# Performance work log

Hardware: AMD Instinct MI355X
Metric: run time of the kernel (lower is better)

Reference implementation:

```python
import jax, jax.numpy as jnp
import numpy as np

B = 4096
LATENT, COND, HIDDEN, OUT, E, GATE_H = 768, 512, 1024, 512, 8, 512
INPUT = LATENT + COND          # 1280
INTER = LATENT + HIDDEN        # 1792
NEG_SLOPE = 0.01
LN_EPS = 1e-5


def _uniform(k, shape, bound):
    return jax.random.uniform(k, shape, jnp.float32, -bound, bound)


def setup_inputs() -> dict:
    key = jax.random.key(0)
    ks = jax.random.split(key, 32)
    inp = {
        'z': jax.random.normal(ks[0], (B, LATENT), jnp.float32),
        'c': jax.random.normal(ks[1], (B, COND), jnp.float32),
    }
    # expert weight/bias stacks, 'origin' init: stdv = 1/sqrt(wdim1)
    dims = [(INPUT, HIDDEN), (INTER, HIDDEN), (INTER, HIDDEN), (INTER, HIDDEN), (INTER, OUT)]
    ki = 2
    for i, (d1, d2) in enumerate(dims):
        stdv = 1.0 / np.sqrt(d1)
        inp[f'w{i}'] = _uniform(ks[ki], (E, d1, d2), stdv); ki += 1
        inp[f'b{i}'] = _uniform(ks[ki], (E, d2), stdv); ki += 1
        # LayerNorm params (torch default: gamma=1, beta=0)
        ln_dim = INPUT if i == 0 else INTER
        inp[f'ln_g{i}'] = jnp.ones((ln_dim,), jnp.float32)
        inp[f'ln_b{i}'] = jnp.zeros((ln_dim,), jnp.float32)
    # gate MLP: Linear(INPUT,GATE_H) -> LeakyReLU -> Linear(GATE_H,GATE_H) -> LeakyReLU -> Linear(GATE_H,E)
    for j, (fi, fo) in enumerate([(INPUT, GATE_H), (GATE_H, GATE_H), (GATE_H, E)]):
        bound = 1.0 / np.sqrt(fi)
        inp[f'gW{j}'] = _uniform(ks[ki], (fi, fo), bound); ki += 1
        inp[f'gb{j}'] = _uniform(ks[ki], (fo,), bound); ki += 1
    return inp


def _layernorm(x, g, b):
    mu = jnp.mean(x, axis=-1, keepdims=True)
    var = jnp.mean(jnp.square(x - mu), axis=-1, keepdims=True)
    return (x - mu) * jax.lax.rsqrt(var + LN_EPS) * g + b


def _mix(coeff, x, w, b):
    # per-sample soft-mixed expert linear: einsum('be,bj,ejk->bk') + einsum('be,ek->bk')
    h = jnp.einsum('bj,ejk->bek', x, w)          # [B,E,K]
    return jnp.einsum('be,bek->bk', coeff, h) + coeff @ b


def reference(z, c, w0, b0, w1, b1, w2, b2, w3, b3, w4, b4,
              ln_g0, ln_b0, ln_g1, ln_b1, ln_g2, ln_b2, ln_g3, ln_b3, ln_g4, ln_b4,
              gW0, gb0, gW1, gb1, gW2, gb2):
    zc = jnp.concatenate([z, c], axis=-1)        # [B, INPUT]
    g = jax.nn.leaky_relu(zc @ gW0 + gb0, NEG_SLOPE)
    g = jax.nn.leaky_relu(g @ gW1 + gb1, NEG_SLOPE)
    coeff = jax.nn.softmax(g @ gW2 + gb2, axis=-1)   # [B, E]

    x = _layernorm(zc, ln_g0, ln_b0)
    layer_out = jax.nn.leaky_relu(_mix(coeff, x, w0, b0), NEG_SLOPE)

    for w, b, lg, lb in [(w1, b1, ln_g1, ln_b1), (w2, b2, ln_g2, ln_b2), (w3, b3, ln_g3, ln_b3)]:
        x = _layernorm(jnp.concatenate([z, layer_out], axis=-1), lg, lb)
        layer_out = jax.nn.leaky_relu(layer_out + _mix(coeff, x, w, b), NEG_SLOPE)

    x = _layernorm(jnp.concatenate([z, layer_out], axis=-1), ln_g4, ln_b4)
    return _mix(coeff, x, w4, b4)                # [B, OUT], no residual/activation
```

## Files before the change

kernel.cpp:

```cpp
#include <hip/hip_runtime.h>


typedef _Float16 f16;
typedef _Float16 f16x8 __attribute__((ext_vector_type(8)));
typedef _Float16 f16x4 __attribute__((ext_vector_type(4)));
typedef float    f32x4 __attribute__((ext_vector_type(4)));

typedef __attribute__((address_space(1))) void as1_void;
typedef __attribute__((address_space(3))) void as3_void;

__device__ __forceinline__ void gload_lds16(const void* g, void* l) {
  __builtin_amdgcn_global_load_lds((as1_void*)g, (as3_void*)l, 16, 0, 0);
}

__device__ __forceinline__ float leaky(float v) { return v > 0.f ? v : 0.01f * v; }

__global__ __launch_bounds__(256) void transpose_cast(const float* __restrict__ in,
                                                      f16* __restrict__ out,
                                                      int R, int C) {
  __shared__ float tile[32][33];
  const size_t mat = (size_t)R * C;
  const float* I = in + mat * blockIdx.z;
  f16* O = out + mat * blockIdx.z;
  const int c0 = blockIdx.x * 32, r0 = blockIdx.y * 32;
  const int tx = threadIdx.x, ty = threadIdx.y;
#pragma unroll
  for (int i = ty; i < 32; i += 8)
    tile[i][tx] = I[(size_t)(r0 + i) * C + (c0 + tx)];
  __syncthreads();
#pragma unroll
  for (int i = ty; i < 32; i += 8)
    O[(size_t)(c0 + i) * R + (r0 + tx)] = (f16)tile[tx][i];
}

__global__ __launch_bounds__(256) void ln0_kernel(
    const float* __restrict__ z, const float* __restrict__ prev,
    const float* __restrict__ gam, const float* __restrict__ bet,
    f16* __restrict__ Xh, f16* __restrict__ raw) {
  constexpr int DP = 512, D = 768 + DP, NCH = D / 4;
  constexpr float invD = 1.f / (float)D;
  const int row = blockIdx.x, tid = threadIdx.x;
  const float4* z4 = (const float4*)(z + (size_t)row * 768);
  const float4* p4 = (const float4*)(prev + (size_t)row * DP);

  float4 v0 = (tid < 192) ? z4[tid] : p4[tid - 192];
  const bool has1 = (tid + 256) < NCH;
  float4 v1 = make_float4(0.f, 0.f, 0.f, 0.f);
  if (has1) v1 = p4[tid + 64];
  float s  = v0.x + v0.y + v0.z + v0.w + v1.x + v1.y + v1.z + v1.w;
  float ss = v0.x * v0.x + v0.y * v0.y + v0.z * v0.z + v0.w * v0.w +
             v1.x * v1.x + v1.y * v1.y + v1.z * v1.z + v1.w * v1.w;
#pragma unroll
  for (int off = 32; off > 0; off >>= 1) {
    s += __shfl_down(s, off);
    ss += __shfl_down(ss, off);
  }
  __shared__ float red[10];
  const int wave = tid >> 6, lane = tid & 63;
  if (lane == 0) { red[wave] = s; red[4 + wave] = ss; }
  __syncthreads();
  if (tid == 0) {
    float S = red[0] + red[1] + red[2] + red[3];
    float SS = red[4] + red[5] + red[6] + red[7];
    float mu = S * invD;
    float var = SS * invD - mu * mu;
    red[8] = mu;
    red[9] = rsqrtf(var + 1e-5f);
  }
  __syncthreads();
  const float mu = red[8], rs = red[9];
  {
    const int c = tid;
    float4 g4 = ((const float4*)gam)[c];
    float4 b4 = ((const float4*)bet)[c];
    f16x4 h;
    h[0] = (f16)((v0.x - mu) * rs * g4.x + b4.x);
    h[1] = (f16)((v0.y - mu) * rs * g4.y + b4.y);
    h[2] = (f16)((v0.z - mu) * rs * g4.z + b4.z);
    h[3] = (f16)((v0.w - mu) * rs * g4.w + b4.w);
    ((f16x4*)Xh)[(size_t)row * NCH + c] = h;
    f16x4 r;
    r[0] = (f16)v0.x; r[1] = (f16)v0.y; r[2] = (f16)v0.z; r[3] = (f16)v0.w;
    ((f16x4*)raw)[(size_t)row * NCH + c] = r;
  }
  if (has1) {
    const int c = tid + 256;
    float4 g4 = ((const float4*)gam)[c];
    float4 b4 = ((const float4*)bet)[c];
    f16x4 h;
    h[0] = (f16)((v1.x - mu) * rs * g4.x + b4.x);
    h[1] = (f16)((v1.y - mu) * rs * g4.y + b4.y);
    h[2] = (f16)((v1.z - mu) * rs * g4.z + b4.z);
    h[3] = (f16)((v1.w - mu) * rs * g4.w + b4.w);
    ((f16x4*)Xh)[(size_t)row * NCH + c] = h;
    f16x4 r;
    r[0] = (f16)v1.x; r[1] = (f16)v1.y; r[2] = (f16)v1.z; r[3] = (f16)v1.w;
    ((f16x4*)raw)[(size_t)row * NCH + c] = r;
  }
}

template <bool HAS_RESID>
__global__ __launch_bounds__(256) void ln_combine_kernel(
    const float* __restrict__ z, const f16* __restrict__ P,
    float* __restrict__ lay,
    const float* __restrict__ gam, const float* __restrict__ bet,
    f16* __restrict__ Xh) {
  constexpr int DP = 1024, D = 768 + DP, NCH = D / 4;
  constexpr size_t PSTRIDE = (size_t)4096 * DP;
  constexpr float invD = 1.f / (float)D;
  const int row = blockIdx.x, tid = threadIdx.x;
  const float4* z4 = (const float4*)(z + (size_t)row * 768);
  float4* lay4 = (float4*)(lay + (size_t)row * DP);

  auto comb = [&](int j) -> float4 {
    float4 v = make_float4(0.f, 0.f, 0.f, 0.f);
#pragma unroll
    for (int zz = 0; zz < 4; ++zz) {
      f16x4 a = ((const f16x4*)(P + PSTRIDE * zz + (size_t)row * DP))[j];
      v.x += (float)a[0]; v.y += (float)a[1]; v.z += (float)a[2]; v.w += (float)a[3];
    }
    if constexpr (HAS_RESID) {
      float4 r = lay4[j];
      v.x += r.x; v.y += r.y; v.z += r.z; v.w += r.w;
    }
    v.x = leaky(v.x); v.y = leaky(v.y); v.z = leaky(v.z); v.w = leaky(v.w);
    return v;
  };

  float4 v0, v1;
  if (tid < 192) {
    v0 = z4[tid];
  } else {
    v0 = comb(tid - 192);
  }
  const bool has1 = tid < 192;
  if (has1) v1 = comb(tid + 64);
  else v1 = make_float4(0.f, 0.f, 0.f, 0.f);

  if (tid >= 192) lay4[tid - 192] = v0;
  if (has1) lay4[tid + 64] = v1;

  float s  = v0.x + v0.y + v0.z + v0.w + v1.x + v1.y + v1.z + v1.w;
  float ss = v0.x * v0.x + v0.y * v0.y + v0.z * v0.z + v0.w * v0.w +
             v1.x * v1.x + v1.y * v1.y + v1.z * v1.z + v1.w * v1.w;
#pragma unroll
  for (int off = 32; off > 0; off >>= 1) {
    s += __shfl_down(s, off);
    ss += __shfl_down(ss, off);
  }
  __shared__ float red[10];
  const int wave = tid >> 6, lane = tid & 63;
  if (lane == 0) { red[wave] = s; red[4 + wave] = ss; }
  __syncthreads();
  if (tid == 0) {
    float S = red[0] + red[1] + red[2] + red[3];
    float SS = red[4] + red[5] + red[6] + red[7];
    float mu = S * invD;
    float var = SS * invD - mu * mu;
    red[8] = mu;
    red[9] = rsqrtf(var + 1e-5f);
  }
  __syncthreads();
  const float mu = red[8], rs = red[9];
  {
    const int c = tid;
    float4 g4 = ((const float4*)gam)[c];
    float4 b4 = ((const float4*)bet)[c];
    f16x4 h;
    h[0] = (f16)((v0.x - mu) * rs * g4.x + b4.x);
    h[1] = (f16)((v0.y - mu) * rs * g4.y + b4.y);
    h[2] = (f16)((v0.z - mu) * rs * g4.z + b4.z);
    h[3] = (f16)((v0.w - mu) * rs * g4.w + b4.w);
    ((f16x4*)Xh)[(size_t)row * NCH + c] = h;
  }
  if (has1) {
    const int c = tid + 256;
    float4 g4 = ((const float4*)gam)[c];
    float4 b4 = ((const float4*)bet)[c];
    f16x4 h;
    h[0] = (f16)((v1.x - mu) * rs * g4.x + b4.x);
    h[1] = (f16)((v1.y - mu) * rs * g4.y + b4.y);
    h[2] = (f16)((v1.z - mu) * rs * g4.z + b4.z);
    h[3] = (f16)((v1.w - mu) * rs * g4.w + b4.w);
    ((f16x4*)Xh)[(size_t)row * NCH + c] = h;
  }
}

__global__ __launch_bounds__(256) void final_combine(const f16* __restrict__ P,
                                                     float* __restrict__ out) {
  constexpr size_t PSTRIDE = (size_t)4096 * 512;
  const int i = blockIdx.x * 256 + threadIdx.x;
  float4 v = make_float4(0.f, 0.f, 0.f, 0.f);
#pragma unroll
  for (int zz = 0; zz < 4; ++zz) {
    f16x4 a = ((const f16x4*)(P + PSTRIDE * zz))[i];
    v.x += (float)a[0]; v.y += (float)a[1]; v.z += (float)a[2]; v.w += (float)a[3];
  }
  ((float4*)out)[i] = v;
}

template <int K>
__global__ __launch_bounds__(256) void gate_gemm(const f16* __restrict__ A,
                                                 const f16* __restrict__ BT,
                                                 const float* __restrict__ bias,
                                                 f16* __restrict__ out) {
  constexpr int N = 512, BK = 64;
  __shared__ f16 sA[128 * BK];
  __shared__ f16 sB[64 * BK];
  const int tid = threadIdx.x, wave = tid >> 6, lane = tid & 63;
  const int quad = lane >> 4, l16 = lane & 15;
  const int wm = (wave >> 1) * 64, wn = (wave & 1) * 32;
  const int row0 = blockIdx.x * 128, col0 = blockIdx.y * 64;
  const int key = (l16 & 7) << 3;

  f32x4 acc[4][2];
#pragma unroll
  for (int ns = 0; ns < 2; ++ns) {
    float bv = bias[col0 + wn + ns * 16 + l16];
    f32x4 b4 = {bv, bv, bv, bv};
#pragma unroll
    for (int ms = 0; ms < 4; ++ms) acc[ms][ns] = b4;
  }
#pragma unroll 1
  for (int k0 = 0; k0 < K; k0 += BK) {
    __syncthreads();
#pragma unroll
    for (int it = 0; it < 4; ++it) {
      int co = ((it * 4 + wave) << 10) | (lane << 4);
      int r = co >> 7;
      int cs = ((((co >> 4) & 7) ^ (r & 7)) << 3);
      gload_lds16(A + (size_t)(row0 + r) * K + (k0 + cs), (char*)sA + co);
    }
#pragma unroll
    for (int it = 0; it < 2; ++it) {
      int co = ((it * 4 + wave) << 10) | (lane << 4);
      int r = co >> 7;
      int cs = ((((co >> 4) & 7) ^ (r & 7)) << 3);
      gload_lds16(BT + (size_t)(col0 + r) * K + (k0 + cs), (char*)sB + co);
    }
    __syncthreads();
#pragma unroll
    for (int kk = 0; kk < BK; kk += 32) {
      f16x8 af[4], bf[2];
#pragma unroll
      for (int ms = 0; ms < 4; ++ms)
        af[ms] = *(const f16x8*)(sA + (wm + ms * 16 + l16) * BK + (((kk + quad * 8)) ^ key));
#pragma unroll
      for (int ns = 0; ns < 2; ++ns)
        bf[ns] = *(const f16x8*)(sB + (wn + ns * 16 + l16) * BK + (((kk + quad * 8)) ^ key));
#pragma unroll
      for (int ms = 0; ms < 4; ++ms)
#pragma unroll
        for (int ns = 0; ns < 2; ++ns)
          acc[ms][ns] = __builtin_amdgcn_mfma_f32_16x16x32_f16(af[ms], bf[ns], acc[ms][ns], 0, 0, 0);
    }
  }
#pragma unroll
  for (int ms = 0; ms < 4; ++ms)
#pragma unroll
    for (int i = 0; i < 4; ++i) {
      const int gr = row0 + wm + ms * 16 + quad * 4 + i;
      f16* op = out + (size_t)gr * N + (col0 + wn + l16);
#pragma unroll
      for (int ns = 0; ns < 2; ++ns) op[ns * 16] = (f16)leaky(acc[ms][ns][i]);
    }
}

__global__ __launch_bounds__(256) void gate_out_softmax(const f16* __restrict__ g2,
                                                        const float* __restrict__ W,
                                                        const float* __restrict__ bias,
                                                        float* __restrict__ coeff) {
  const int wave = threadIdx.x >> 6, lane = threadIdx.x & 63;
  const int row = blockIdx.x * 4 + wave;
  float acc[8] = {0.f, 0.f, 0.f, 0.f, 0.f, 0.f, 0.f, 0.f};
  const f16* xr = g2 + (size_t)row * 512;
#pragma unroll
  for (int j = 0; j < 8; ++j) {
    int k = lane + 64 * j;
    float x = (float)xr[k];
    const float4* wp = (const float4*)(W + k * 8);
    float4 w0 = wp[0], w1 = wp[1];
    acc[0] += x * w0.x; acc[1] += x * w0.y; acc[2] += x * w0.z; acc[3] += x * w0.w;
    acc[4] += x * w1.x; acc[5] += x * w1.y; acc[6] += x * w1.z; acc[7] += x * w1.w;
  }
#pragma unroll
  for (int off = 32; off > 0; off >>= 1) {
#pragma unroll
    for (int e = 0; e < 8; ++e) acc[e] += __shfl_xor(acc[e], off);
  }
  float m = -1e30f;
#pragma unroll
  for (int e = 0; e < 8; ++e) { acc[e] += bias[e]; m = fmaxf(m, acc[e]); }
  float s = 0.f;
#pragma unroll
  for (int e = 0; e < 8; ++e) { acc[e] = __expf(acc[e] - m); s += acc[e]; }
  const float inv = 1.f / s;
  if (lane == 0) {
    float* cp = coeff + (size_t)row * 8;
#pragma unroll
    for (int e = 0; e < 8; ++e) cp[e] = acc[e] * inv;
  }
}

template <int K, int NTOT, int NB>
__global__ __launch_bounds__(256) void mix_gemm(const f16* __restrict__ X,
                                                const f16* __restrict__ WT,
                                                const float* __restrict__ bias,
                                                const float* __restrict__ coeff,
                                                f16* __restrict__ P) {
  constexpr int BK = 64, KH = K / 4;
  constexpr int NSUB = NB / 32;
  constexpr int BISS = (NB * BK * 2) / 4096;
  __shared__ f16 sA[128 * BK];
  __shared__ f16 sB[NB * BK];
  __shared__ float sCoef[128 * 8];

  const int tid = threadIdx.x, wave = tid >> 6, lane = tid & 63;
  const int quad = lane >> 4, l16 = lane & 15;
  const int wm = (wave >> 1) * 64, wn = (wave & 1) * (NB / 2);
  const int row0 = blockIdx.x * 128, col0 = blockIdx.y * NB;
  const int kb = blockIdx.z * KH;
  const int key = (l16 & 7) << 3;

#pragma unroll
  for (int i = tid; i < 128 * 8; i += 256)
    sCoef[i] = coeff[(size_t)(row0 + (i >> 3)) * 8 + (i & 7)];

  f32x4 accM[4][NSUB];
  {
    f32x4 zz = {0.f, 0.f, 0.f, 0.f};
#pragma unroll
    for (int ms = 0; ms < 4; ++ms)
#pragma unroll
      for (int ns = 0; ns < NSUB; ++ns) accM[ms][ns] = zz;
  }

#pragma unroll 1
  for (int e = 0; e < 8; ++e) {
    f32x4 accE[4][NSUB];
#pragma unroll
    for (int ns = 0; ns < NSUB; ++ns) {
      float bv = (blockIdx.z == 0) ? bias[(size_t)e * NTOT + col0 + wn + ns * 16 + l16] : 0.f;
      f32x4 b4 = {bv, bv, bv, bv};
#pragma unroll
      for (int ms = 0; ms < 4; ++ms) accE[ms][ns] = b4;
    }
    const f16* Be = WT + (size_t)e * NTOT * K;
#pragma unroll 1
    for (int k0 = 0; k0 < KH; k0 += BK) {
      __syncthreads();
#pragma unroll
      for (int it = 0; it < 4; ++it) {
        int co = ((it * 4 + wave) << 10) | (lane << 4);
        int r = co >> 7;
        int cs = ((((co >> 4) & 7) ^ (r & 7)) << 3);
        gload_lds16(X + (size_t)(row0 + r) * K + (kb + k0 + cs), (char*)sA + co);
      }
#pragma unroll
      for (int it = 0; it < BISS; ++it) {
        int co = ((it * 4 + wave) << 10) | (lane << 4);
        int r = co >> 7;
        int cs = ((((co >> 4) & 7) ^ (r & 7)) << 3);
        gload_lds16(Be + (size_t)(col0 + r) * K + (kb + k0 + cs), (char*)sB + co);
      }
      __syncthreads();
#pragma unroll
      for (int kk = 0; kk < BK; kk += 32) {
        f16x8 af[4], bf[NSUB];
#pragma unroll
        for (int ms = 0; ms < 4; ++ms)
          af[ms] = *(const f16x8*)(sA + (wm + ms * 16 + l16) * BK + (((kk + quad * 8)) ^ key));
#pragma unroll
        for (int ns = 0; ns < NSUB; ++ns)
          bf[ns] = *(const f16x8*)(sB + (wn + ns * 16 + l16) * BK + (((kk + quad * 8)) ^ key));
#pragma unroll
        for (int ms = 0; ms < 4; ++ms)
#pragma unroll
          for (int ns = 0; ns < NSUB; ++ns)
            accE[ms][ns] = __builtin_amdgcn_mfma_f32_16x16x32_f16(af[ms], bf[ns], accE[ms][ns], 0, 0, 0);
      }
    }
#pragma unroll
    for (int ms = 0; ms < 4; ++ms) {
      const int rb = wm + ms * 16 + quad * 4;
      float c0 = sCoef[(rb + 0) * 8 + e];
      float c1 = sCoef[(rb + 1) * 8 + e];
      float c2 = sCoef[(rb + 2) * 8 + e];
      float c3 = sCoef[(rb + 3) * 8 + e];
#pragma unroll
      for (int ns = 0; ns < NSUB; ++ns) {
        accM[ms][ns][0] += c0 * accE[ms][ns][0];
        accM[ms][ns][1] += c1 * accE[ms][ns][1];
        accM[ms][ns][2] += c2 * accE[ms][ns][2];
        accM[ms][ns][3] += c3 * accE[ms][ns][3];
      }
    }
  }
  f16* Pz = P + (size_t)blockIdx.z * 4096 * NTOT;
#pragma unroll
  for (int ms = 0; ms < 4; ++ms)
#pragma unroll
    for (int i = 0; i < 4; ++i) {
      const int gr = row0 + wm + ms * 16 + quad * 4 + i;
      f16* orow = Pz + (size_t)gr * NTOT + (col0 + wn + l16);
#pragma unroll
      for (int ns = 0; ns < NSUB; ++ns) orow[ns * 16] = (f16)accM[ms][ns][i];
    }
}

extern "C" void kernel_launch(void* const* d_in, const int* in_sizes, int n_in,
                              void* d_out, int out_size, void* d_ws, size_t ws_size,
                              hipStream_t stream) {
  const float* z = (const float*)d_in[0];
  const float* c = (const float*)d_in[1];
  const float* w[5]   = {(const float*)d_in[2], (const float*)d_in[6], (const float*)d_in[10],
                         (const float*)d_in[14], (const float*)d_in[18]};
  const float* bb[5]  = {(const float*)d_in[3], (const float*)d_in[7], (const float*)d_in[11],
                         (const float*)d_in[15], (const float*)d_in[19]};
  const float* lng[5] = {(const float*)d_in[4], (const float*)d_in[8], (const float*)d_in[12],
                         (const float*)d_in[16], (const float*)d_in[20]};
  const float* lnb[5] = {(const float*)d_in[5], (const float*)d_in[9], (const float*)d_in[13],
                         (const float*)d_in[17], (const float*)d_in[21]};
  const float* gW0 = (const float*)d_in[22];
  const float* gb0 = (const float*)d_in[23];
  const float* gW1 = (const float*)d_in[24];
  const float* gb1 = (const float*)d_in[25];
  const float* gW2 = (const float*)d_in[26];
  const float* gb2 = (const float*)d_in[27];
  float* outF = (float*)d_out;

  char* ws = (char*)d_ws;
  f16*   WT    = (f16*)(ws + 0);
  f16*   gT0   = (f16*)(ws + 29360128);
  f16*   gT1   = (f16*)(ws + 30670848);
  f16*   Xh    = (f16*)(ws + 31195136);
  float* coeff = (float*)(ws + 45875200);
  float* lay   = (float*)(ws + 46006272);
  f16*   zc_h  = (f16*)(ws + 62783488);
  f16*   g1h   = (f16*)(ws + 73269248);
  f16*   g2h   = (f16*)(ws + 77463552);
  f16*   P     = (f16*)(ws + 62783488);

  const dim3 tb(32, 8, 1);

  transpose_cast<<<dim3(16, 40, 1), tb, 0, stream>>>(gW0, gT0, 1280, 512);
  transpose_cast<<<dim3(16, 16, 1), tb, 0, stream>>>(gW1, gT1, 512, 512);

  ln0_kernel<<<4096, 256, 0, stream>>>(z, c, lng[0], lnb[0], Xh, zc_h);

  gate_gemm<1280><<<dim3(32, 8), 256, 0, stream>>>(zc_h, gT0, gb0, g1h);
  gate_gemm<512><<<dim3(32, 8), 256, 0, stream>>>(g1h, gT1, gb1, g2h);
  gate_out_softmax<<<1024, 256, 0, stream>>>(g2h, gW2, gb2, coeff);

  transpose_cast<<<dim3(32, 40, 8), tb, 0, stream>>>(w[0], WT, 1280, 1024);
  mix_gemm<1280, 1024, 128><<<dim3(32, 8, 4), 256, 0, stream>>>(Xh, WT, bb[0], coeff, P);
  ln_combine_kernel<false><<<4096, 256, 0, stream>>>(z, P, lay, lng[1], lnb[1], Xh);

  for (int i = 1; i <= 3; ++i) {
    transpose_cast<<<dim3(32, 56, 8), tb, 0, stream>>>(w[i], WT, 1792, 1024);
    mix_gemm<1792, 1024, 128><<<dim3(32, 8, 4), 256, 0, stream>>>(Xh, WT, bb[i], coeff, P);
    const int nl = (i < 3) ? i + 1 : 4;
    ln_combine_kernel<true><<<4096, 256, 0, stream>>>(z, P, lay, lng[nl], lnb[nl], Xh);
  }

  transpose_cast<<<dim3(16, 56, 8), tb, 0, stream>>>(w[4], WT, 1792, 512);
  mix_gemm<1792, 512, 64><<<dim3(32, 8, 4), 256, 0, stream>>>(Xh, WT, bb[4], coeff, P);
  final_combine<<<2048, 256, 0, stream>>>(P, outF);

  (void)in_sizes; (void)n_in; (void)out_size; (void)ws_size;
}
```

Before: 1.135 ms.

## Fold gate coefficients into A operand and reuse A tile across experts

```diff
diff --git a/kernel.cpp b/kernel.cpp
--- a/kernel.cpp
+++ b/kernel.cpp
@@ -115,7 +115,7 @@
   auto comb = [&](int j) -> float4 {
     float4 v = make_float4(0.f, 0.f, 0.f, 0.f);
 #pragma unroll
-    for (int zz = 0; zz < 4; ++zz) {
+    for (int zz = 0; zz < 2; ++zz) {
       f16x4 a = ((const f16x4*)(P + PSTRIDE * zz + (size_t)row * DP))[j];
       v.x += (float)a[0]; v.y += (float)a[1]; v.z += (float)a[2]; v.w += (float)a[3];
     }
@@ -192,7 +192,7 @@
   const int i = blockIdx.x * 256 + threadIdx.x;
   float4 v = make_float4(0.f, 0.f, 0.f, 0.f);
 #pragma unroll
-  for (int zz = 0; zz < 4; ++zz) {
+  for (int zz = 0; zz < 2; ++zz) {
     f16x4 a = ((const f16x4*)(P + PSTRIDE * zz))[i];
     v.x += (float)a[0]; v.y += (float)a[1]; v.z += (float)a[2]; v.w += (float)a[3];
   }
@@ -308,12 +308,13 @@
                                                 const float* __restrict__ bias,
                                                 const float* __restrict__ coeff,
                                                 f16* __restrict__ P) {
-  constexpr int BK = 64, KH = K / 4;
+  constexpr int BK = 64, KH = K / 2;
   constexpr int NSUB = NB / 32;
   constexpr int BISS = (NB * BK * 2) / 4096;
   __shared__ f16 sA[128 * BK];
-  __shared__ f16 sB[NB * BK];
-  __shared__ float sCoef[128 * 8];
+  __shared__ f16 sB[2][NB * BK];
+  __shared__ f16 sCoefH[128 * 8];
+  __shared__ f16 sBiasH[8 * NB];
 
   const int tid = threadIdx.x, wave = tid >> 6, lane = tid & 63;
   const int quad = lane >> 4, l16 = lane & 15;
@@ -322,9 +323,30 @@
   const int kb = blockIdx.z * KH;
   const int key = (l16 & 7) << 3;
 
-#pragma unroll
   for (int i = tid; i < 128 * 8; i += 256)
-    sCoef[i] = coeff[(size_t)(row0 + (i >> 3)) * 8 + (i & 7)];
+    sCoefH[i] = (f16)coeff[(size_t)(row0 + (i >> 3)) * 8 + (i & 7)];
+  for (int i = tid; i < 8 * NB; i += 256)
+    sBiasH[i] = (f16)bias[(size_t)(i / NB) * NTOT + col0 + (i % NB)];
+
+  auto stageA = [&](int k0) {
+#pragma unroll
+    for (int it = 0; it < 4; ++it) {
+      int co = ((it * 4 + wave) << 10) | (lane << 4);
+      int r = co >> 7;
+      int cs = ((((co >> 4) & 7) ^ (r & 7)) << 3);
+      gload_lds16(X + (size_t)(row0 + r) * K + (kb + k0 + cs), (char*)sA + co);
+    }
+  };
+  auto stageB = [&](int e, int k0, int b) {
+    const f16* Be = WT + (size_t)e * NTOT * K;
+#pragma unroll
+    for (int it = 0; it < BISS; ++it) {
+      int co = ((it * 4 + wave) << 10) | (lane << 4);
+      int r = co >> 7;
+      int cs = ((((co >> 4) & 7) ^ (r & 7)) << 3);
+      gload_lds16(Be + (size_t)(col0 + r) * K + (kb + k0 + cs), (char*)sB[b] + co);
+    }
+  };
 
   f32x4 accM[4][NSUB];
   {
@@ -335,76 +357,74 @@
       for (int ns = 0; ns < NSUB; ++ns) accM[ms][ns] = zz;
   }
 
+  f16x8 af[2][4];
+  stageA(0);
+  stageB(0, 0, 0);
+  int buf = 0;
+
 #pragma unroll 1
-  for (int e = 0; e < 8; ++e) {
-    f32x4 accE[4][NSUB];
-#pragma unroll
-    for (int ns = 0; ns < NSUB; ++ns) {
-      float bv = (blockIdx.z == 0) ? bias[(size_t)e * NTOT + col0 + wn + ns * 16 + l16] : 0.f;
-      f32x4 b4 = {bv, bv, bv, bv};
-#pragma unroll
-      for (int ms = 0; ms < 4; ++ms) accE[ms][ns] = b4;
-    }
-    const f16* Be = WT + (size_t)e * NTOT * K;
+  for (int k0 = 0; k0 < KH; k0 += BK) {
 #pragma unroll 1
-    for (int k0 = 0; k0 < KH; k0 += BK) {
+    for (int e = 0; e < 8; ++e) {
       __syncthreads();
-#pragma unroll
-      for (int it = 0; it < 4; ++it) {
-        int co = ((it * 4 + wave) << 10) | (lane << 4);
-        int r = co >> 7;
-        int cs = ((((co >> 4) & 7) ^ (r & 7)) << 3);
-        gload_lds16(X + (size_t)(row0 + r) * K + (kb + k0 + cs), (char*)sA + co);
+      if (e < 7)                stageB(e + 1, k0, buf ^ 1);
+      else if (k0 + BK < KH)    stageB(0, k0 + BK, buf ^ 1);
+      if (e == 1 && k0 + BK < KH) stageA(k0 + BK);
+      if (e == 0) {
+#pragma unroll
+        for (int kk = 0; kk < 2; ++kk)
+#pragma unroll
+          for (int ms = 0; ms < 4; ++ms)
+            af[kk][ms] = *(const f16x8*)(sA + (wm + ms * 16 + l16) * BK +
+                                         ((kk * 32 + quad * 8) ^ key));
       }
-#pragma unroll
-      for (int it = 0; it < BISS; ++it) {
-        int co = ((it * 4 + wave) << 10) | (lane << 4);
-        int r = co >> 7;
-        int cs = ((((co >> 4) & 7) ^ (r & 7)) << 3);
-        gload_lds16(Be + (size_t)(col0 + r) * K + (kb + k0 + cs), (char*)sB + co);
+      f16 ce[4];
+#pragma unroll
+      for (int ms = 0; ms < 4; ++ms)
+        ce[ms] = sCoefH[(wm + ms * 16 + l16) * 8 + e];
+#pragma unroll
+      for (int kk = 0; kk < 2; ++kk) {
+        f16x8 bf[NSUB];
+#pragma unroll
+        for (int ns = 0; ns < NSUB; ++ns)
+          bf[ns] = *(const f16x8*)(sB[buf] + (wn + ns * 16 + l16) * BK +
+                                   ((kk * 32 + quad * 8) ^ key));
+#pragma unroll
+        for (int ms = 0; ms < 4; ++ms) {
+          f16x8 as;
+#pragma unroll
+          for (int j = 0; j < 8; ++j) as[j] = af[kk][ms][j] * ce[ms];
+#pragma unroll
+          for (int ns = 0; ns < NSUB; ++ns)
+            accM[ms][ns] = __builtin_amdgcn_mfma_f32_16x16x32_f16(as, bf[ns], accM[ms][ns], 0, 0, 0);
+        }
       }
-      __syncthreads();
-#pragma unroll
-      for (int kk = 0; kk < BK; kk += 32) {
-        f16x8 af[4], bf[NSUB];
-#pragma unroll
-        for (int ms = 0; ms < 4; ++ms)
-          af[ms] = *(const f16x8*)(sA + (wm + ms * 16 + l16) * BK + (((kk + quad * 8)) ^ key));
-#pragma unroll
-        for (int ns = 0; ns < NSUB; ++ns)
-          bf[ns] = *(const f16x8*)(sB + (wn + ns * 16 + l16) * BK + (((kk + quad * 8)) ^ key));
-#pragma unroll
-        for (int ms = 0; ms < 4; ++ms)
-#pragma unroll
-          for (int ns = 0; ns < NSUB; ++ns)
-            accE[ms][ns] = __builtin_amdgcn_mfma_f32_16x16x32_f16(af[ms], bf[ns], accE[ms][ns], 0, 0, 0);
+      buf ^= 1;
+    }
+  }
+
+  const bool addB = (blockIdx.z == 0);
+  f16* Pz = P + (size_t)blockIdx.z * 4096 * NTOT;
+#pragma unroll
+  for (int ms = 0; ms < 4; ++ms)
+#pragma unroll
+    for (int i = 0; i < 4; ++i) {
+      const int lr = wm + ms * 16 + quad * 4 + i;
+      const int gr = row0 + lr;
+      f16x8 ch = *(const f16x8*)(sCoefH + lr * 8);
+      f16* orow = Pz + (size_t)gr * NTOT + (col0 + wn + l16);
+#pragma unroll
+      for (int ns = 0; ns < NSUB; ++ns) {
+        float v = accM[ms][ns][i];
+        if (addB) {
+          float bsum = 0.f;
+#pragma unroll
+          for (int e = 0; e < 8; ++e)
+            bsum += (float)ch[e] * (float)sBiasH[e * NB + wn + ns * 16 + l16];
+          v += bsum;
+        }
+        orow[ns * 16] = (f16)v;
       }
-    }
-#pragma unroll
-    for (int ms = 0; ms < 4; ++ms) {
-      const int rb = wm + ms * 16 + quad * 4;
-      float c0 = sCoef[(rb + 0) * 8 + e];
-      float c1 = sCoef[(rb + 1) * 8 + e];
-      float c2 = sCoef[(rb + 2) * 8 + e];
-      float c3 = sCoef[(rb + 3) * 8 + e];
-#pragma unroll
-      for (int ns = 0; ns < NSUB; ++ns) {
-        accM[ms][ns][0] += c0 * accE[ms][ns][0];
-        accM[ms][ns][1] += c1 * accE[ms][ns][1];
-        accM[ms][ns][2] += c2 * accE[ms][ns][2];
-        accM[ms][ns][3] += c3 * accE[ms][ns][3];
-      }
-    }
-  }
-  f16* Pz = P + (size_t)blockIdx.z * 4096 * NTOT;
-#pragma unroll
-  for (int ms = 0; ms < 4; ++ms)
-#pragma unroll
-    for (int i = 0; i < 4; ++i) {
-      const int gr = row0 + wm + ms * 16 + quad * 4 + i;
-      f16* orow = Pz + (size_t)gr * NTOT + (col0 + wn + l16);
-#pragma unroll
-      for (int ns = 0; ns < NSUB; ++ns) orow[ns * 16] = (f16)accM[ms][ns][i];
     }
 }
 
@@ -453,18 +473,18 @@
   gate_out_softmax<<<1024, 256, 0, stream>>>(g2h, gW2, gb2, coeff);
 
   transpose_cast<<<dim3(32, 40, 8), tb, 0, stream>>>(w[0], WT, 1280, 1024);
-  mix_gemm<1280, 1024, 128><<<dim3(32, 8, 4), 256, 0, stream>>>(Xh, WT, bb[0], coeff, P);
+  mix_gemm<1280, 1024, 128><<<dim3(32, 8, 2), 256, 0, stream>>>(Xh, WT, bb[0], coeff, P);
   ln_combine_kernel<false><<<4096, 256, 0, stream>>>(z, P, lay, lng[1], lnb[1], Xh);
 
   for (int i = 1; i <= 3; ++i) {
     transpose_cast<<<dim3(32, 56, 8), tb, 0, stream>>>(w[i], WT, 1792, 1024);
-    mix_gemm<1792, 1024, 128><<<dim3(32, 8, 4), 256, 0, stream>>>(Xh, WT, bb[i], coeff, P);
+    mix_gemm<1792, 1024, 128><<<dim3(32, 8, 2), 256, 0, stream>>>(Xh, WT, bb[i], coeff, P);
     const int nl = (i < 3) ? i + 1 : 4;
     ln_combine_kernel<true><<<4096, 256, 0, stream>>>(z, P, lay, lng[nl], lnb[nl], Xh);
   }
 
   transpose_cast<<<dim3(16, 56, 8), tb, 0, stream>>>(w[4], WT, 1792, 512);
-  mix_gemm<1792, 512, 64><<<dim3(32, 8, 4), 256, 0, stream>>>(Xh, WT, bb[4], coeff, P);
+  mix_gemm<1792, 512, 64><<<dim3(32, 8, 2), 256, 0, stream>>>(Xh, WT, bb[4], coeff, P);
   final_combine<<<2048, 256, 0, stream>>>(P, outF);
 
   (void)in_sizes; (void)n_in; (void)out_size; (void)ws_size;
```

Measured after the change: 955.1 us. 1.19x faster.
